# Kernel optimization log

Hardware: AMD Instinct MI355X
Metric: run time of the kernel (lower is better)

## Reference

```python
import jax, jax.numpy as jnp
import numpy as np

N, E, IN, OUT, EF = 20000, 100000, 32, 32, 16
NEG = -1e30  # finite sentinel for masked scores (avoids inf*0 grads)


def setup_inputs() -> dict:
    key = jax.random.key(0)
    ks = jax.random.split(key, 8)
    return {
        "feat": jax.random.normal(ks[0], (N, IN), jnp.float32),
        "efeat": jax.random.normal(ks[1], (E, EF), jnp.float32),
        "src": jax.random.randint(ks[2], (E,), 0, N, dtype=jnp.int32),
        "dst": jax.random.randint(ks[3], (E,), 0, N, dtype=jnp.int32),
        "etype": jax.random.randint(ks[4], (E,), 0, 2, dtype=jnp.int32),
        "attn_w": jax.random.normal(ks[5], (2 * IN, 1), jnp.float32) * 0.1,
        "attn_b": jnp.zeros((1,), jnp.float32),
        "ef1_w": jax.random.normal(ks[6], (EF, IN * OUT), jnp.float32) * 0.05,
        "ef1_b": jnp.zeros((IN * OUT,), jnp.float32),
        "ef2_w": jax.random.normal(ks[7], (EF, IN * OUT), jnp.float32) * 0.05,
        "ef2_b": jnp.zeros((IN * OUT,), jnp.float32),
        "bias": jnp.zeros((OUT,), jnp.float32),
    }


def reference(feat, efeat, src, dst, etype, attn_w, attn_b,
              ef1_w, ef1_b, ef2_w, ef2_b, bias):
    n_nodes = feat.shape[0]
    z_src = feat[src]                      # [E, IN] gather src features
    z_dst = feat[dst]                      # [E, IN] gather dst features
    # per-edge scalar attention score: leaky_relu(Linear(cat(z_src, z_dst)))
    score = jax.nn.leaky_relu(
        (jnp.concatenate([z_src, z_dst], axis=1) @ attn_w + attn_b)[:, 0]
    )  # [E]

    def relation_agg(mask, w, b):
        # edge-specific weight matrices: [E, IN, OUT]
        We = (efeat @ w + b).reshape(E, IN, OUT)
        # message per edge = src_feat @ W_e  (sum over IN commutes with attn)
        msg = jnp.einsum('ei,eio->eo', z_src, We)        # [E, OUT]
        # segment softmax over incoming edges of this relation per dst node
        s = jnp.where(mask, score, NEG)
        smax = jax.ops.segment_max(s, dst, num_segments=n_nodes)
        ex = jnp.where(mask, jnp.exp(s - smax[dst]), 0.0)
        den = jax.ops.segment_sum(ex, dst, num_segments=n_nodes)
        alpha = ex / jnp.where(den > 0, den, 1.0)[dst]   # [E]
        # attention-weighted scatter-sum to dst nodes
        return jax.ops.segment_sum(alpha[:, None] * msg, dst,
                                   num_segments=n_nodes)  # [N, OUT]

    rst = relation_agg(etype == 0, ef1_w, ef1_b) \
        + relation_agg(etype == 1, ef2_w, ef2_b) \
        + bias
    return rst
```

## Files before the change

kernel.cpp:

```cpp
#include <hip/hip_runtime.h>

typedef __attribute__((ext_vector_type(8))) short bf16x8;
typedef __attribute__((ext_vector_type(16))) float f32x16;
typedef __attribute__((ext_vector_type(2))) float f32x2;

__device__ __forceinline__ unsigned short f2b(float x) {
    unsigned u = __float_as_uint(x);
    unsigned r = (u + 0x7fffu + ((u >> 16) & 1u)) >> 16;
    return (unsigned short)r;
}
__device__ __forceinline__ unsigned f2b2(float lo, float hi) {
    return (unsigned)f2b(lo) | ((unsigned)f2b(hi) << 16);
}
__device__ __forceinline__ float b2f(unsigned short u) {
    return __uint_as_float((unsigned)u << 16);
}
__device__ __forceinline__ f32x2 pk_fma(f32x2 a, f32x2 b, f32x2 c) {
    f32x2 d;
    asm("v_pk_fma_f32 %0, %1, %2, %3" : "=v"(d) : "v"(a), "v"(b), "v"(c));
    return d;
}

__global__ void k_zero(int* __restrict__ hist, int* __restrict__ lkb,
                       const float* __restrict__ feat, const float* __restrict__ attn_w,
                       const float* __restrict__ w1, const float* __restrict__ b1,
                       const float* __restrict__ w2, const float* __restrict__ b2,
                       float* __restrict__ ps, float* __restrict__ pd,
                       unsigned short* __restrict__ PA, int N) {
    int idx = blockIdx.x * blockDim.x + threadIdx.x;
    int n2q = (2 * N + 3) >> 2;
    if (idx < n2q) ((int4*)hist)[idx] = make_int4(0, 0, 0, 0);
    if (idx < 16) ((int4*)lkb)[idx] = make_int4(0, 0, 0, 0);
    if (idx < N) {
        const float4* zp = (const float4*)(feat + (long)idx * 32);
        const float4* aw = (const float4*)attn_w;
        float a = 0.f, b = 0.f;
        #pragma unroll
        for (int j = 0; j < 8; ++j) {
            float4 z = zp[j], wa = aw[j], wb = aw[8 + j];
            a = fmaf(z.x, wa.x, a); a = fmaf(z.y, wa.y, a);
            a = fmaf(z.z, wa.z, a); a = fmaf(z.w, wa.w, a);
            b = fmaf(z.x, wb.x, b); b = fmaf(z.y, wb.y, b);
            b = fmaf(z.z, wb.z, b); b = fmaf(z.w, wb.w, b);
        }
        ps[idx] = a; pd[idx] = b;
    }
    if (idx < 2 * 17 * 2 * 64) {
        int l = idx & 63;
        int x = idx >> 6;
        int h = x & 1; x >>= 1;
        int t = x % 17;
        int r = x / 17;
        const float* W = r ? w2 : w1;
        const float* B = r ? b2 : b1;
        int o = l & 31;
        int kb = h * 16 + (l >> 5) * 8;
        unsigned short v[8];
        #pragma unroll
        for (int j = 0; j < 8; ++j) {
            int i = kb + j;
            float sv = (t < 16) ? W[t * 1024 + i * 32 + o] : B[i * 32 + o];
            v[j] = f2b(sv);
        }
        uint4 pack;
        pack.x = (unsigned)v[0] | ((unsigned)v[1] << 16);
        pack.y = (unsigned)v[2] | ((unsigned)v[3] << 16);
        pack.z = (unsigned)v[4] | ((unsigned)v[5] << 16);
        pack.w = (unsigned)v[6] | ((unsigned)v[7] << 16);
        *((uint4*)PA + idx) = pack;
    }
}

__global__ void k_hist2(const int* __restrict__ src, const int* __restrict__ dst,
                        const int* __restrict__ etype,
                        const float* __restrict__ ps, const float* __restrict__ pd,
                        const float* __restrict__ attn_b,
                        int* __restrict__ hist, int* __restrict__ key,
                        float* __restrict__ exu, int E, int N) {
    int e = blockIdx.x * blockDim.x + threadIdx.x;
    if (e >= E) return;
    int d = dst[e];
    int k = etype[e] * N + d;
    float sc = ps[src[e]] + pd[d] + attn_b[0];
    sc = sc >= 0.f ? sc : 0.01f * sc;
    key[e] = k;
    exu[e] = __expf(sc);
    atomicAdd(&hist[k], 1);
}

__global__ __launch_bounds__(256) void k_scan(const int* __restrict__ hist,
                                              int* __restrict__ rowptr,
                                              int* __restrict__ cursor,
                                              int* __restrict__ lkb, int n, int E) {
    __shared__ int s[256];
    __shared__ int soff;
    int t = threadIdx.x, b = blockIdx.x;
    int i0 = b * 1024 + t * 4;
    int4 hv = make_int4(0, 0, 0, 0);
    if (i0 + 3 < n) hv = *(const int4*)(hist + i0);
    else {
        if (i0 + 0 < n) hv.x = hist[i0 + 0];
        if (i0 + 1 < n) hv.y = hist[i0 + 1];
        if (i0 + 2 < n) hv.z = hist[i0 + 2];
        if (i0 + 3 < n) hv.w = hist[i0 + 3];
    }
    int tot = hv.x + hv.y + hv.z + hv.w;
    s[t] = tot;
    __syncthreads();
    for (int d = 1; d < 256; d <<= 1) {
        int x = (t >= d) ? s[t - d] : 0;
        __syncthreads();
        s[t] += x;
        __syncthreads();
    }
    if (t == 255) atomicExch(&lkb[b], s[255] + 1);
    if (t < 64) {
        int v = 0;
        if (t < b) {
            int p;
            do { p = atomicAdd(&lkb[t], 0); } while (p == 0);
            v = p - 1;
        }
        #pragma unroll
        for (int d = 32; d >= 1; d >>= 1) v += __shfl_down(v, d);
        if (t == 0) soff = v;
    }
    __syncthreads();
    int run = s[t] - tot + soff;
    if (i0 + 0 < n) { rowptr[i0 + 0] = run; cursor[i0 + 0] = run; } run += hv.x;
    if (i0 + 1 < n) { rowptr[i0 + 1] = run; cursor[i0 + 1] = run; } run += hv.y;
    if (i0 + 2 < n) { rowptr[i0 + 2] = run; cursor[i0 + 2] = run; } run += hv.z;
    if (i0 + 3 < n) { rowptr[i0 + 3] = run; cursor[i0 + 3] = run; }
    if (t == 0 && b == 0) rowptr[n] = E;
}

__global__ void k_scatter(const int* __restrict__ key, const float* __restrict__ exu,
                          int* __restrict__ cursor, int* __restrict__ sortidx,
                          float* __restrict__ exs, int E) {
    int e = blockIdx.x * blockDim.x + threadIdx.x;
    if (e >= E) return;
    int pos = atomicAdd(&cursor[key[e]], 1);
    sortidx[pos] = e;
    exs[pos] = exu[e];
}

__global__ __launch_bounds__(256) void k_msg(
    const float* __restrict__ feat, const float* __restrict__ efeat,
    const int* __restrict__ src, const unsigned short* __restrict__ PA,
    const int* __restrict__ sortidx, const int* __restrict__ rowptr,
    unsigned short* __restrict__ wmsg, int E, int N) {
    int cnt0 = rowptr[N];
    int cnt1 = E - cnt0;
    int nb0 = (cnt0 + 127) >> 7;
    int bi = blockIdx.x;
    int r, base, count, relstart;
    if (bi < nb0) { r = 0; base = bi * 128; count = cnt0; relstart = 0; }
    else {
        r = 1; base = (bi - nb0) * 128; count = cnt1; relstart = cnt0;
        if (base >= count) return;
    }

    int tid = threadIdx.x;
    int lane = tid & 63;
    int ecol = (tid >> 6) * 32 + (lane & 31);
    int kb = (lane >> 5) * 8;
    int gi = base + ecol;
    bool valid = gi < count;
    int e = sortidx[relstart + min(gi, count - 1)];
    int sn = src[e];

    const float4* zp = (const float4*)(feat + (long)sn * 32);
    float4 z0 = zp[kb >> 2], z1 = zp[(kb >> 2) + 1];
    float4 z2 = zp[(kb >> 2) + 4], z3 = zp[(kb >> 2) + 5];
    uint4 pb0, pb1;
    pb0.x = f2b2(z0.x, z0.y); pb0.y = f2b2(z0.z, z0.w);
    pb0.z = f2b2(z1.x, z1.y); pb0.w = f2b2(z1.z, z1.w);
    pb1.x = f2b2(z2.x, z2.y); pb1.y = f2b2(z2.z, z2.w);
    pb1.z = f2b2(z3.x, z3.y); pb1.w = f2b2(z3.z, z3.w);
    bf16x8 b0 = *(bf16x8*)&pb0, b1 = *(bf16x8*)&pb1;

    const float4* up = (const float4*)(efeat + (long)e * 16);
    float4 u0 = up[0], u1 = up[1], u2 = up[2], u3 = up[3];
    float uu[16] = { u0.x, u0.y, u0.z, u0.w, u1.x, u1.y, u1.z, u1.w,
                     u2.x, u2.y, u2.z, u2.w, u3.x, u3.y, u3.z, u3.w };

    const bf16x8* pa = (const bf16x8*)PA + (long)r * 34 * 64 + lane;

    f32x2 m2[8];
    {
        bf16x8 a0 = pa[32 * 64];
        bf16x8 a1 = pa[33 * 64];
        f32x16 c;
        #pragma unroll
        for (int k = 0; k < 16; ++k) c[k] = 0.f;
        c = __builtin_amdgcn_mfma_f32_32x32x16_bf16(a0, b0, c, 0, 0, 0);
        c = __builtin_amdgcn_mfma_f32_32x32x16_bf16(a1, b1, c, 0, 0, 0);
        #pragma unroll
        for (int k = 0; k < 8; ++k) { m2[k][0] = c[2 * k]; m2[k][1] = c[2 * k + 1]; }
    }
    #pragma unroll 4
    for (int t = 0; t < 16; ++t) {
        bf16x8 a0 = pa[(t * 2 + 0) * 64];
        bf16x8 a1 = pa[(t * 2 + 1) * 64];
        f32x16 c;
        #pragma unroll
        for (int k = 0; k < 16; ++k) c[k] = 0.f;
        c = __builtin_amdgcn_mfma_f32_32x32x16_bf16(a0, b0, c, 0, 0, 0);
        c = __builtin_amdgcn_mfma_f32_32x32x16_bf16(a1, b1, c, 0, 0, 0);
        f32x2 ud; ud[0] = uu[t]; ud[1] = uu[t];
        #pragma unroll
        for (int k = 0; k < 8; ++k) {
            f32x2 cc; cc[0] = c[2 * k]; cc[1] = c[2 * k + 1];
            m2[k] = pk_fma(ud, cc, m2[k]);
        }
    }

    if (valid) {
        unsigned short* wr = wmsg + (long)(relstart + gi) * 32 + kb / 2;
        *(uint2*)(wr +  0) = make_uint2(f2b2(m2[0][0], m2[0][1]), f2b2(m2[1][0], m2[1][1]));
        *(uint2*)(wr +  8) = make_uint2(f2b2(m2[2][0], m2[2][1]), f2b2(m2[3][0], m2[3][1]));
        *(uint2*)(wr + 16) = make_uint2(f2b2(m2[4][0], m2[4][1]), f2b2(m2[5][0], m2[5][1]));
        *(uint2*)(wr + 24) = make_uint2(f2b2(m2[6][0], m2[6][1]), f2b2(m2[7][0], m2[7][1]));
    }
}

__global__ void k_reduce(const int* __restrict__ rowptr, const float* __restrict__ exs,
                         const unsigned short* __restrict__ wmsg,
                         const float* __restrict__ bias,
                         float* __restrict__ out, int N) {
    int tid = blockIdx.x * blockDim.x + threadIdx.x;
    if (tid >= N * 8) return;
    int n = tid >> 3, og = tid & 7;
    float4 acc = ((const float4*)bias)[og];
    #pragma unroll 1
    for (int r = 0; r < 2; ++r) {
        int k = r * N + n;
        int s = rowptr[k], e2 = rowptr[k + 1];
        if (s >= e2) continue;
        float den = 0.f;
        #pragma unroll 1
        for (int p = s; p < e2; ++p) den += exs[p];
        float inv = 1.f / den;
        #pragma unroll 1
        for (int p = s; p < e2; ++p) {
            float w = exs[p] * inv;
            ushort4 m = *(const ushort4*)(wmsg + (long)p * 32 + og * 4);
            acc.x = fmaf(w, b2f(m.x), acc.x);
            acc.y = fmaf(w, b2f(m.y), acc.y);
            acc.z = fmaf(w, b2f(m.z), acc.z);
            acc.w = fmaf(w, b2f(m.w), acc.w);
        }
    }
    ((float4*)out)[tid] = acc;
}

extern "C" void kernel_launch(void* const* d_in, const int* in_sizes, int n_in,
                              void* d_out, int out_size, void* d_ws, size_t ws_size,
                              hipStream_t stream) {
    const float* feat   = (const float*)d_in[0];
    const float* efeat  = (const float*)d_in[1];
    const int*   src    = (const int*)d_in[2];
    const int*   dst    = (const int*)d_in[3];
    const int*   etype  = (const int*)d_in[4];
    const float* attn_w = (const float*)d_in[5];
    const float* attn_b = (const float*)d_in[6];
    const float* ef1_w  = (const float*)d_in[7];
    const float* ef1_b  = (const float*)d_in[8];
    const float* ef2_w  = (const float*)d_in[9];
    const float* ef2_b  = (const float*)d_in[10];
    const float* bias   = (const float*)d_in[11];

    int E = in_sizes[2];
    int N = in_sizes[0] / 32;
    int n2 = 2 * N;
    int nb = (n2 + 1023) / 1024;

    float*          ps      = (float*)d_ws;
    float*          pd      = ps + N;
    unsigned short* PA      = (unsigned short*)(pd + N);
    int*            hist    = (int*)(PA + 2 * 17 * 2 * 64 * 8);
    int*            rowptr  = hist + n2;
    int*            cursor  = rowptr + n2 + 1;
    int*            lkb     = cursor + n2;
    int*            keyb    = lkb + 64;
    float*          exu     = (float*)(keyb + E);
    int*            sortidx = (int*)(exu + E);
    float*          exs     = (float*)(sortidx + E);
    unsigned short* wmsg    = (unsigned short*)(((size_t)(exs + E) + 15) & ~(size_t)15);
    float*          out     = (float*)d_out;

    k_zero<<<(N + 255) / 256, 256, 0, stream>>>(hist, lkb, feat, attn_w,
                                                ef1_w, ef1_b, ef2_w, ef2_b,
                                                ps, pd, PA, N);
    k_hist2<<<(E + 255) / 256, 256, 0, stream>>>(src, dst, etype, ps, pd, attn_b,
                                                 hist, keyb, exu, E, N);
    k_scan<<<nb, 256, 0, stream>>>(hist, rowptr, cursor, lkb, n2, E);
    k_scatter<<<(E + 255) / 256, 256, 0, stream>>>(keyb, exu, cursor, sortidx, exs, E);
    k_msg<<<(E + 127) / 128 + 2, 256, 0, stream>>>(feat, efeat, src, PA, sortidx,
                                                   rowptr, wmsg, E, N);
    k_reduce<<<(N * 8 + 255) / 256, 256, 0, stream>>>(rowptr, exs, wmsg, bias, out, N);
}
```

Measured before the change: 51.85 us.

## Fuse edge scatter into message kernel and compute both relations per wave

Removes the separate scatter kernel and the sortidx array. The message kernel now walks edges in their original order, takes each edge's sorted slot with an atomic on the cursor, and writes the message there directly. Because a wave can now hold edges of both relations, it runs the MFMAs for both relation weight sets and selects per lane. This saves one launch and the sortidx round-trip but doubles the MFMA work and turns the message stores into scattered writes instead of sequential ones.

```diff
diff --git a/kernel.cpp b/kernel.cpp
--- a/kernel.cpp
+++ b/kernel.cpp
@@ -134,40 +134,32 @@
     if (t == 0 && b == 0) rowptr[n] = E;
 }
 
-__global__ void k_scatter(const int* __restrict__ key, const float* __restrict__ exu,
-                          int* __restrict__ cursor, int* __restrict__ sortidx,
-                          float* __restrict__ exs, int E) {
-    int e = blockIdx.x * blockDim.x + threadIdx.x;
-    if (e >= E) return;
-    int pos = atomicAdd(&cursor[key[e]], 1);
-    sortidx[pos] = e;
-    exs[pos] = exu[e];
-}
-
-__global__ __launch_bounds__(256) void k_msg(
+__global__ __launch_bounds__(256) void k_scatmsg(
     const float* __restrict__ feat, const float* __restrict__ efeat,
     const int* __restrict__ src, const unsigned short* __restrict__ PA,
-    const int* __restrict__ sortidx, const int* __restrict__ rowptr,
+    const int* __restrict__ key, const float* __restrict__ exu,
+    int* __restrict__ cursor, float* __restrict__ exs,
     unsigned short* __restrict__ wmsg, int E, int N) {
-    int cnt0 = rowptr[N];
-    int cnt1 = E - cnt0;
-    int nb0 = (cnt0 + 127) >> 7;
-    int bi = blockIdx.x;
-    int r, base, count, relstart;
-    if (bi < nb0) { r = 0; base = bi * 128; count = cnt0; relstart = 0; }
-    else {
-        r = 1; base = (bi - nb0) * 128; count = cnt1; relstart = cnt0;
-        if (base >= count) return;
-    }
-
     int tid = threadIdx.x;
     int lane = tid & 63;
     int ecol = (tid >> 6) * 32 + (lane & 31);
-    int kb = (lane >> 5) * 8;
-    int gi = base + ecol;
-    bool valid = gi < count;
-    int e = sortidx[relstart + min(gi, count - 1)];
-    int sn = src[e];
+    int hi = lane >> 5;
+    int kb = hi * 8;
+    int e = blockIdx.x * 128 + ecol;
+    bool valid = e < E;
+    int ec = min(e, E - 1);
+
+    int k = key[ec];
+    float ex = exu[ec];
+    int r = (k >= N) ? 1 : 0;
+    int sn = src[ec];
+
+    int pos = 0;
+    if (hi == 0 && valid) {
+        pos = atomicAdd(&cursor[k], 1);
+        exs[pos] = ex;
+    }
+    pos = __shfl(pos, lane & 31);
 
     const float4* zp = (const float4*)(feat + (long)sn * 32);
     float4 z0 = zp[kb >> 2], z1 = zp[(kb >> 2) + 1];
@@ -179,44 +171,51 @@
     pb1.z = f2b2(z3.x, z3.y); pb1.w = f2b2(z3.z, z3.w);
     bf16x8 b0 = *(bf16x8*)&pb0, b1 = *(bf16x8*)&pb1;
 
-    const float4* up = (const float4*)(efeat + (long)e * 16);
+    const float4* up = (const float4*)(efeat + (long)ec * 16);
     float4 u0 = up[0], u1 = up[1], u2 = up[2], u3 = up[3];
     float uu[16] = { u0.x, u0.y, u0.z, u0.w, u1.x, u1.y, u1.z, u1.w,
                      u2.x, u2.y, u2.z, u2.w, u3.x, u3.y, u3.z, u3.w };
 
-    const bf16x8* pa = (const bf16x8*)PA + (long)r * 34 * 64 + lane;
+    const bf16x8* pa0 = (const bf16x8*)PA + lane;
+    const bf16x8* pa1 = (const bf16x8*)PA + 34 * 64 + lane;
+    bool sel1 = (r == 1);
 
     f32x2 m2[8];
     {
-        bf16x8 a0 = pa[32 * 64];
-        bf16x8 a1 = pa[33 * 64];
-        f32x16 c;
-        #pragma unroll
-        for (int k = 0; k < 16; ++k) c[k] = 0.f;
-        c = __builtin_amdgcn_mfma_f32_32x32x16_bf16(a0, b0, c, 0, 0, 0);
-        c = __builtin_amdgcn_mfma_f32_32x32x16_bf16(a1, b1, c, 0, 0, 0);
-        #pragma unroll
-        for (int k = 0; k < 8; ++k) { m2[k][0] = c[2 * k]; m2[k][1] = c[2 * k + 1]; }
-    }
-    #pragma unroll 4
+        f32x16 c0, c1;
+        #pragma unroll
+        for (int q = 0; q < 16; ++q) { c0[q] = 0.f; c1[q] = 0.f; }
+        c0 = __builtin_amdgcn_mfma_f32_32x32x16_bf16(pa0[32 * 64], b0, c0, 0, 0, 0);
+        c0 = __builtin_amdgcn_mfma_f32_32x32x16_bf16(pa0[33 * 64], b1, c0, 0, 0, 0);
+        c1 = __builtin_amdgcn_mfma_f32_32x32x16_bf16(pa1[32 * 64], b0, c1, 0, 0, 0);
+        c1 = __builtin_amdgcn_mfma_f32_32x32x16_bf16(pa1[33 * 64], b1, c1, 0, 0, 0);
+        #pragma unroll
+        for (int q = 0; q < 8; ++q) {
+            m2[q][0] = sel1 ? c1[2 * q]     : c0[2 * q];
+            m2[q][1] = sel1 ? c1[2 * q + 1] : c0[2 * q + 1];
+        }
+    }
+    #pragma unroll 2
     for (int t = 0; t < 16; ++t) {
-        bf16x8 a0 = pa[(t * 2 + 0) * 64];
-        bf16x8 a1 = pa[(t * 2 + 1) * 64];
-        f32x16 c;
-        #pragma unroll
-        for (int k = 0; k < 16; ++k) c[k] = 0.f;
-        c = __builtin_amdgcn_mfma_f32_32x32x16_bf16(a0, b0, c, 0, 0, 0);
-        c = __builtin_amdgcn_mfma_f32_32x32x16_bf16(a1, b1, c, 0, 0, 0);
+        f32x16 c0, c1;
+        #pragma unroll
+        for (int q = 0; q < 16; ++q) { c0[q] = 0.f; c1[q] = 0.f; }
+        c0 = __builtin_amdgcn_mfma_f32_32x32x16_bf16(pa0[(t * 2 + 0) * 64], b0, c0, 0, 0, 0);
+        c0 = __builtin_amdgcn_mfma_f32_32x32x16_bf16(pa0[(t * 2 + 1) * 64], b1, c0, 0, 0, 0);
+        c1 = __builtin_amdgcn_mfma_f32_32x32x16_bf16(pa1[(t * 2 + 0) * 64], b0, c1, 0, 0, 0);
+        c1 = __builtin_amdgcn_mfma_f32_32x32x16_bf16(pa1[(t * 2 + 1) * 64], b1, c1, 0, 0, 0);
         f32x2 ud; ud[0] = uu[t]; ud[1] = uu[t];
         #pragma unroll
-        for (int k = 0; k < 8; ++k) {
-            f32x2 cc; cc[0] = c[2 * k]; cc[1] = c[2 * k + 1];
-            m2[k] = pk_fma(ud, cc, m2[k]);
+        for (int q = 0; q < 8; ++q) {
+            f32x2 cc;
+            cc[0] = sel1 ? c1[2 * q]     : c0[2 * q];
+            cc[1] = sel1 ? c1[2 * q + 1] : c0[2 * q + 1];
+            m2[q] = pk_fma(ud, cc, m2[q]);
         }
     }
 
     if (valid) {
-        unsigned short* wr = wmsg + (long)(relstart + gi) * 32 + kb / 2;
+        unsigned short* wr = wmsg + (long)pos * 32 + kb / 2;
         *(uint2*)(wr +  0) = make_uint2(f2b2(m2[0][0], m2[0][1]), f2b2(m2[1][0], m2[1][1]));
         *(uint2*)(wr +  8) = make_uint2(f2b2(m2[2][0], m2[2][1]), f2b2(m2[3][0], m2[3][1]));
         *(uint2*)(wr + 16) = make_uint2(f2b2(m2[4][0], m2[4][1]), f2b2(m2[5][0], m2[5][1]));
@@ -284,8 +283,7 @@
     int*            lkb     = cursor + n2;
     int*            keyb    = lkb + 64;
     float*          exu     = (float*)(keyb + E);
-    int*            sortidx = (int*)(exu + E);
-    float*          exs     = (float*)(sortidx + E);
+    float*          exs     = (float*)(exu + E);
     unsigned short* wmsg    = (unsigned short*)(((size_t)(exs + E) + 15) & ~(size_t)15);
     float*          out     = (float*)d_out;
 
@@ -295,8 +293,7 @@
     k_hist2<<<(E + 255) / 256, 256, 0, stream>>>(src, dst, etype, ps, pd, attn_b,
                                                  hist, keyb, exu, E, N);
     k_scan<<<nb, 256, 0, stream>>>(hist, rowptr, cursor, lkb, n2, E);
-    k_scatter<<<(E + 255) / 256, 256, 0, stream>>>(keyb, exu, cursor, sortidx, exs, E);
-    k_msg<<<(E + 127) / 128 + 2, 256, 0, stream>>>(feat, efeat, src, PA, sortidx,
-                                                   rowptr, wmsg, E, N);
+    k_scatmsg<<<(E + 127) / 128, 256, 0, stream>>>(feat, efeat, src, PA, keyb, exu,
+                                                   cursor, exs, wmsg, E, N);
     k_reduce<<<(N * 8 + 255) / 256, 256, 0, stream>>>(rowptr, exs, wmsg, bias, out, N);
 }
```

Measured after the change: 58.71 us. 1.13x slower.
